# Kernel tuning notes

Measured on AMD Instinct MI355X. Metric: run time of the kernel, lower is better.

Reference implementation:

```python
import jax, jax.numpy as jnp
import numpy as np

VOCAB = 100000
EMBED_DIM = 300
TOPK = 10
BATCH = 1024


def setup_inputs() -> dict:
    key = jax.random.key(0)
    k1, k2 = jax.random.split(key)
    wordid = jax.random.randint(k1, (BATCH,), 0, VOCAB, dtype=jnp.int64 if jax.config.jax_enable_x64 else jnp.int32)
    weight = jax.random.normal(k2, (VOCAB, EMBED_DIM), dtype=jnp.float32)
    return {"wordid": wordid, "weight": weight}


def reference(wordid, weight):
    # Embedding lookup: [B, D]
    wordvec = weight[wordid]
    # Dense similarity against full vocab: [B, V]
    sim = jnp.einsum('bd,vd->bv', wordvec, weight)
    # top-(k+1), sorted descending; drop column 0 (the query word itself)
    score, indice = jax.lax.top_k(sim, TOPK + 1)
    return score[:, 1:], indice[:, 1:]
```

## Files before the change

kernel.cpp:

```cpp
#include <hip/hip_runtime.h>
#include <math.h>

#define BATCH 1024
#define VOCAB 100000
#define KDIM  300
#define TOPK  10

#define NKB    10
#define NCB_B  6272
#define NCB_A  64
#define NCC    392
#define NCAND  (NCC*8)
#define NKF    24
#define NDOT   (NKF*4)

typedef __attribute__((ext_vector_type(8))) short bf16x8;
typedef __attribute__((ext_vector_type(4))) float f32x4;
typedef unsigned long long u64;

#define GL2LDS(gsrc, ldst)                                                    \
    __builtin_amdgcn_global_load_lds(                                         \
        (const __attribute__((address_space(1))) void*)(gsrc),                \
        (__attribute__((address_space(3))) void*)(ldst), 16, 0, 0)

__device__ __forceinline__ ushort f2bf(float f) {
    union { float f; unsigned u; } v; v.f = f;
    unsigned r = v.u + 0x7FFFu + ((v.u >> 16) & 1u);
    return (ushort)(r >> 16);
}

__device__ __forceinline__ void ins4(int (&l)[4], int e) {
    if (e <= l[3]) return;
    bool g0 = e > l[0], g1 = e > l[1], g2 = e > l[2];
    l[3] = g2 ? l[2] : e;
    l[2] = g2 ? (g1 ? l[1] : e) : l[2];
    l[1] = g1 ? (g0 ? l[0] : e) : l[1];
    l[0] = g0 ? e : l[0];
}

template<int N>
__device__ __forceinline__ void pins64(u64 (&ks)[N], u64 k) {
    if (k <= ks[N-1]) return;
    #pragma unroll
    for (int p = N-1; p >= 0; --p) {
        bool gt  = k > ks[p];
        bool gtp = (p > 0) ? (k > ks[p-1]) : false;
        ks[p] = gt ? (gtp ? ks[p-1] : k) : ks[p];
    }
}

__global__ __launch_bounds__(256)
void convert_frags(const int* __restrict__ wordid, const float* __restrict__ weight,
                   ushort* __restrict__ ws_b, ushort* __restrict__ ws_a, int nb4)
{
    const int t   = threadIdx.x;
    const int w   = t >> 6, l = t & 63;
    const int bid = blockIdx.x;
    const bool is_a = (bid >= nb4);
    const int cb  = (is_a ? (bid - nb4) : bid) * 4 + w;
    ushort* dst = is_a ? ws_a : ws_b;
    const int kstride = is_a ? 64 : NCB_B;

    const int r16  = l & 15;
    const int ksub = (l >> 4) * 8;

    const int row = is_a ? wordid[cb*16 + r16] : (cb*16 + r16);
    const bool vr = (row < VOCAB);
    const float* src = weight + (size_t)(vr ? row : 0) * KDIM;

    #pragma unroll
    for (int kb = 0; kb < NKB; ++kb) {
        const int k0 = kb*32 + ksub;
        float4 a = make_float4(0.f,0.f,0.f,0.f);
        float4 b = make_float4(0.f,0.f,0.f,0.f);
        if (vr) {
            if (k0 + 8 <= KDIM) {
                a = *reinterpret_cast<const float4*>(src + k0);
                b = *reinterpret_cast<const float4*>(src + k0 + 4);
            } else if (k0 + 4 <= KDIM) {
                a = *reinterpret_cast<const float4*>(src + k0);
            }
        }
        uint4 o;
        o.x = (unsigned)f2bf(a.x) | ((unsigned)f2bf(a.y) << 16);
        o.y = (unsigned)f2bf(a.z) | ((unsigned)f2bf(a.w) << 16);
        o.z = (unsigned)f2bf(b.x) | ((unsigned)f2bf(b.y) << 16);
        o.w = (unsigned)f2bf(b.z) | ((unsigned)f2bf(b.w) << 16);
        *reinterpret_cast<uint4*>(&dst[((size_t)kb*kstride + cb)*512 + (size_t)l*8]) = o;
    }
}

__global__ __launch_bounds__(512, 2)
void sim_gemm(const ushort* __restrict__ ws_a, const ushort* __restrict__ ws_b,
              unsigned* __restrict__ cand)
{
    __shared__ __align__(16) char pool[131072];

    const int id = blockIdx.x;
    const int cc = (id & 7) + ((id >> 5) << 3);
    const int rc = (id >> 3) & 3;

    const int t    = threadIdx.x;
    const int wid  = t >> 6, lane = t & 63;
    const int wm   = wid >> 2, wn = wid & 3;
    const int l16  = lane & 15, lk = lane >> 4;

    auto stage_slot = [&](int kt, int slot, int buf) {
        char* ldst = pool + buf*65536 + slot*1024;
        const ushort* src;
        if (slot < 32) {
            src = ws_a + (((size_t)(kt*2 + (slot>>4))*64) + rc*16 + (slot & 15))*512
                       + (size_t)lane*8;
        } else {
            int s2 = slot - 32;
            src = ws_b + (((size_t)(kt*2 + (s2>>4))*NCB_B) + cc*16 + (s2 & 15))*512
                       + (size_t)lane*8;
        }
        GL2LDS(src, (ushort*)ldst);
    };

    f32x4 acc[8][4] = {};

    #pragma unroll
    for (int j = 0; j < 8; ++j) stage_slot(0, wid*8 + j, 0);
    asm volatile("s_waitcnt vmcnt(0)" ::: "memory");
    __builtin_amdgcn_s_barrier();
    asm volatile("" ::: "memory");

    for (int kt = 0; kt < 5; ++kt) {
        const int buf = kt & 1;
        const ushort* Ab = (const ushort*)(pool + buf*65536);
        const ushort* Bb = (const ushort*)(pool + buf*65536 + 32768);

        if (kt < 4) {
            #pragma unroll
            for (int j = 0; j < 8; ++j)
                stage_slot(kt + 1, wid*8 + j, buf ^ 1);
        }

        bf16x8 bfr[2][4];
        #pragma unroll
        for (int kb = 0; kb < 2; ++kb)
            #pragma unroll
            for (int nf = 0; nf < 4; ++nf)
                bfr[kb][nf] = *reinterpret_cast<const bf16x8*>(
                    Bb + (size_t)(kb*16 + wn*4 + nf)*512 + lane*8);

        #pragma unroll
        for (int p = 0; p < 4; ++p) {
            bf16x8 af[2][2];
            #pragma unroll
            for (int kb = 0; kb < 2; ++kb)
                #pragma unroll
                for (int m2 = 0; m2 < 2; ++m2)
                    af[kb][m2] = *reinterpret_cast<const bf16x8*>(
                        Ab + (size_t)(kb*16 + wm*8 + p*2 + m2)*512 + lane*8);

            __builtin_amdgcn_s_setprio(1);
            #pragma unroll
            for (int m2 = 0; m2 < 2; ++m2)
                #pragma unroll
                for (int nf = 0; nf < 4; ++nf) {
                    acc[p*2+m2][nf] = __builtin_amdgcn_mfma_f32_16x16x32_bf16(
                        bfr[0][nf], af[0][m2], acc[p*2+m2][nf], 0, 0, 0);
                    acc[p*2+m2][nf] = __builtin_amdgcn_mfma_f32_16x16x32_bf16(
                        bfr[1][nf], af[1][m2], acc[p*2+m2][nf], 0, 0, 0);
                }
            __builtin_amdgcn_s_setprio(0);
        }

        if (kt < 4) {
            asm volatile("s_waitcnt vmcnt(0)" ::: "memory");
            __builtin_amdgcn_s_barrier();
            asm volatile("" ::: "memory");
        }
    }

    __syncthreads();
    int* Cls = (int*)pool;
    #pragma unroll
    for (int mf = 0; mf < 8; ++mf) {
        int k0 = 0, k1 = 0;
        #pragma unroll
        for (int nf = 0; nf < 4; ++nf) {
            float qm = fmaxf(fmaxf(acc[mf][nf][0], acc[mf][nf][1]),
                             fmaxf(acc[mf][nf][2], acc[mf][nf][3]));
            int key = (int)((__float_as_uint(qm) & 0xFFFF0000u)
                            | (unsigned)(wn*16 + nf*4 + lk));
            if (key > k0)      { k1 = k0; k0 = key; }
            else if (key > k1) { k1 = key; }
        }
        int row = wm*128 + mf*16 + l16;
        int ent = wn*4 + lk;
        Cls[row*33 + ent*2 + 0] = k0;
        Cls[row*33 + ent*2 + 1] = k1;
    }
    __syncthreads();

    {
        int row  = t >> 1, half = t & 1;
        int ks[4] = {0, 0, 0, 0};
        #pragma unroll
        for (int j = 0; j < 16; ++j)
            ins4(ks, Cls[row*33 + half*16 + j]);
        int grow = rc*256 + row;
        size_t base = (size_t)grow*NCAND + cc*8 + half*4;
        *reinterpret_cast<uint4*>(&cand[base]) =
            make_uint4((unsigned)ks[0], (unsigned)ks[1],
                       (unsigned)ks[2], (unsigned)ks[3]);
    }
}

__global__ __launch_bounds__(256, 4)
void topk_finalize(const unsigned* __restrict__ cand, const int* __restrict__ wordid,
                   const float* __restrict__ weight, float* __restrict__ out)
{
    __shared__ u64    Wv[4*NKF];
    __shared__ int    Qq[NKF];
    __shared__ float  Qrow[304];
    __shared__ double Rs[NDOT];
    __shared__ int    Rc[NDOT];

    const int row  = blockIdx.x;
    const int t    = threadIdx.x;
    const int wid  = t >> 6, lane = t & 63;

    if (t < 75)
        *reinterpret_cast<float4*>(&Qrow[t*4]) =
            *reinterpret_cast<const float4*>(weight + (size_t)wordid[row]*KDIM + t*4);

    u64 a[13];
    #pragma unroll
    for (int i = 0; i < 13; ++i) a[i] = 0ull;

    const unsigned* rc = cand + (size_t)row*NCAND;
    #pragma unroll
    for (int i = 0; i < 13; ++i) {
        int off = i*64 + lane;
        if (off < 784) {
            int c = wid*784 + off;
            unsigned e = rc[c];
            u64 comb = ((u64)(e ^ 0x80000000u) << 32)
                     | (unsigned)(((c >> 3) << 6) | (e & 63u));
            pins64<13>(a, comb);
        }
    }

    u64 mywin = 0ull;
    for (int k = 0; k < NKF; ++k) {
        u64 h = a[0], r = h;
        #pragma unroll
        for (int m = 1; m < 64; m <<= 1) {
            u64 o = __shfl_xor(r, m);
            r = (o > r) ? o : r;
        }
        bool win = (h == r);
        #pragma unroll
        for (int j = 0; j < 12; ++j) a[j] = win ? a[j+1] : a[j];
        a[12] = win ? 0ull : a[12];
        mywin = (lane == k) ? r : mywin;
    }
    if (lane < NKF) Wv[wid*NKF + lane] = mywin;
    __syncthreads();

    if (wid == 0) {
        u64 b0 = Wv[lane];
        u64 b1 = (lane < 32) ? Wv[lane + 64] : 0ull;
        if (b1 > b0) { u64 tmp = b0; b0 = b1; b1 = tmp; }

        u64 fin = 0ull;
        for (int k = 0; k < NKF; ++k) {
            u64 h = b0, r = h;
            #pragma unroll
            for (int m = 1; m < 64; m <<= 1) {
                u64 o = __shfl_xor(r, m);
                r = (o > r) ? o : r;
            }
            bool win = (h == r);
            b0 = win ? b1 : b0;
            b1 = win ? 0ull : b1;
            fin = (lane == k) ? r : fin;
        }
        if (lane < NKF) Qq[lane] = (int)(fin & 0xffffffffull);
    }
    __syncthreads();

    {
        const int g = t >> 4, l = t & 15;
        for (int ci = g; ci < NDOT; ci += 16) {
            const int q   = Qq[ci >> 2];
            const int col = q*4 + (ci & 3);
            const bool valid = (col < VOCAB);
            const float* wr = weight + (size_t)(valid ? col : 0)*KDIM;

            double a0 = 0.0, a1 = 0.0;
            #pragma unroll
            for (int k = 0; k < 4; ++k) {
                int sl = (l + 16*k) * 4;
                float4 qa = *reinterpret_cast<const float4*>(&Qrow[sl]);
                float4 wb = *reinterpret_cast<const float4*>(wr + sl);
                a0 += (double)qa.x * wb.x + (double)qa.z * wb.z;
                a1 += (double)qa.y * wb.y + (double)qa.w * wb.w;
            }
            if (l < 11) {
                int sl = (l + 64) * 4;
                float4 qa = *reinterpret_cast<const float4*>(&Qrow[sl]);
                float4 wb = *reinterpret_cast<const float4*>(wr + sl);
                a0 += (double)qa.x * wb.x + (double)qa.z * wb.z;
                a1 += (double)qa.y * wb.y + (double)qa.w * wb.w;
            }
            double s = a0 + a1;
            #pragma unroll
            for (int m = 1; m < 16; m <<= 1) s += __shfl_xor(s, m);
            if (l == 0) { Rs[ci] = valid ? s : -1e300; Rc[ci] = valid ? col : 0x7fffffff; }
        }
    }
    __syncthreads();

    if (wid == 0) {
        double v0 = -INFINITY, v1 = -INFINITY;
        int    c0 = 0x7fffffff, c1 = 0x7fffffff;
        if (lane < NDOT/2) {
            v0 = Rs[lane*2];     c0 = Rc[lane*2];
            v1 = Rs[lane*2 + 1]; c1 = Rc[lane*2 + 1];
        }
        for (int kk = 0; kk < TOPK + 1; ++kk) {
            bool sel = (v0 > v1) || (v0 == v1 && c0 < c1);
            double bv = sel ? v0 : v1;
            int    bc = sel ? c0 : c1;
            #pragma unroll
            for (int m = 1; m < 64; m <<= 1) {
                double ov = __shfl_xor(bv, m);
                int    oc = __shfl_xor(bc, m);
                if (ov > bv || (ov == bv && oc < bc)) { bv = ov; bc = oc; }
            }
            if (kk >= 1 && lane == 0) {
                out[(size_t)row*TOPK + (kk-1)] = (float)bv;
                out[(size_t)BATCH*TOPK + (size_t)row*TOPK + (kk-1)] = (float)bc;
            }
            if (c0 == bc) v0 = -INFINITY;
            if (c1 == bc) v1 = -INFINITY;
        }
    }
}

extern "C" void kernel_launch(void* const* d_in, const int* in_sizes, int n_in,
                              void* d_out, int out_size, void* d_ws, size_t ws_size,
                              hipStream_t stream) {
    const int*   wordid = (const int*)d_in[0];
    const float* weight = (const float*)d_in[1];
    float* out = (float*)d_out;

    const size_t SZ_B = (size_t)NCB_B * NKB * 64 * 16;
    const size_t SZ_A = (size_t)NCB_A * NKB * 64 * 16;

    char* p = (char*)d_ws;
    ushort*   ws_b = (ushort*)p;  p += SZ_B;
    ushort*   ws_a = (ushort*)p;  p += SZ_A;
    unsigned* cand = (unsigned*)p;

    convert_frags<<<NCB_B/4 + NCB_A/4, 256, 0, stream>>>(wordid, weight, ws_b, ws_a, NCB_B/4);
    sim_gemm<<<NCC*4, 512, 0, stream>>>(ws_a, ws_b, cand);
    topk_finalize<<<BATCH, 256, 0, stream>>>(cand, wordid, weight, out);
}
```

Before: 155.1 us.

## Run sim_gemm with 1024-thread blocks, halving per-wave M tile

The GEMM block grows from 8 to 16 waves covering the same 256x256 tile, so each wave owns 64 rows instead of 128 and holds half as many accumulators. Staging is split so each wave issues 4 LDS loads per k-step instead of 8, and the epilogue row mapping is adjusted. The aim is more waves to hide LDS and global latency with lower register pressure. The cost is lower per-wave reuse of B fragments, which means more LDS reads per MFMA and heavier barriers. With 128KB of LDS per block, only one block fits per CU, where before there were two 512-thread blocks.

```diff
diff --git a/kernel.cpp b/kernel.cpp
--- a/kernel.cpp
+++ b/kernel.cpp
@@ -90,7 +90,7 @@
     }
 }
 
-__global__ __launch_bounds__(512, 2)
+__global__ __launch_bounds__(1024)
 void sim_gemm(const ushort* __restrict__ ws_a, const ushort* __restrict__ ws_b,
               unsigned* __restrict__ cand)
 {
@@ -105,24 +105,27 @@
     const int wm   = wid >> 2, wn = wid & 3;
     const int l16  = lane & 15, lk = lane >> 4;
 
-    auto stage_slot = [&](int kt, int slot, int buf) {
-        char* ldst = pool + buf*65536 + slot*1024;
-        const ushort* src;
-        if (slot < 32) {
-            src = ws_a + (((size_t)(kt*2 + (slot>>4))*64) + rc*16 + (slot & 15))*512
-                       + (size_t)lane*8;
-        } else {
-            int s2 = slot - 32;
-            src = ws_b + (((size_t)(kt*2 + (s2>>4))*NCB_B) + cc*16 + (s2 & 15))*512
-                       + (size_t)lane*8;
-        }
-        GL2LDS(src, (ushort*)ldst);
+    auto stage = [&](int kt, int buf) {
+        #pragma unroll
+        for (int j = 0; j < 4; ++j) {
+            const int slot = wid*4 + j;
+            char* ldst = pool + buf*65536 + slot*1024;
+            const ushort* src;
+            if (slot < 32) {
+                src = ws_a + ((size_t)(kt*2 + (slot>>4))*64 + rc*16 + (slot & 15))*512
+                           + (size_t)lane*8;
+            } else {
+                int s2 = slot - 32;
+                src = ws_b + ((size_t)(kt*2 + (s2>>4))*NCB_B + cc*16 + (s2 & 15))*512
+                           + (size_t)lane*8;
+            }
+            GL2LDS(src, (ushort*)ldst);
+        }
     };
 
-    f32x4 acc[8][4] = {};
-
-    #pragma unroll
-    for (int j = 0; j < 8; ++j) stage_slot(0, wid*8 + j, 0);
+    f32x4 acc[4][4] = {};
+
+    stage(0, 0);
     asm volatile("s_waitcnt vmcnt(0)" ::: "memory");
     __builtin_amdgcn_s_barrier();
     asm volatile("" ::: "memory");
@@ -132,40 +135,27 @@
         const ushort* Ab = (const ushort*)(pool + buf*65536);
         const ushort* Bb = (const ushort*)(pool + buf*65536 + 32768);
 
-        if (kt < 4) {
-            #pragma unroll
-            for (int j = 0; j < 8; ++j)
-                stage_slot(kt + 1, wid*8 + j, buf ^ 1);
-        }
-
-        bf16x8 bfr[2][4];
-        #pragma unroll
-        for (int kb = 0; kb < 2; ++kb)
+        if (kt < 4) stage(kt + 1, buf ^ 1);
+
+        #pragma unroll
+        for (int kb = 0; kb < 2; ++kb) {
+            bf16x8 bfr[4], af[4];
             #pragma unroll
             for (int nf = 0; nf < 4; ++nf)
-                bfr[kb][nf] = *reinterpret_cast<const bf16x8*>(
+                bfr[nf] = *reinterpret_cast<const bf16x8*>(
                     Bb + (size_t)(kb*16 + wn*4 + nf)*512 + lane*8);
-
-        #pragma unroll
-        for (int p = 0; p < 4; ++p) {
-            bf16x8 af[2][2];
-            #pragma unroll
-            for (int kb = 0; kb < 2; ++kb)
+            #pragma unroll
+            for (int mf = 0; mf < 4; ++mf)
+                af[mf] = *reinterpret_cast<const bf16x8*>(
+                    Ab + (size_t)(kb*16 + wm*4 + mf)*512 + lane*8);
+
+            __builtin_amdgcn_s_setprio(1);
+            #pragma unroll
+            for (int mf = 0; mf < 4; ++mf)
                 #pragma unroll
-                for (int m2 = 0; m2 < 2; ++m2)
-                    af[kb][m2] = *reinterpret_cast<const bf16x8*>(
-                        Ab + (size_t)(kb*16 + wm*8 + p*2 + m2)*512 + lane*8);
-
-            __builtin_amdgcn_s_setprio(1);
-            #pragma unroll
-            for (int m2 = 0; m2 < 2; ++m2)
-                #pragma unroll
-                for (int nf = 0; nf < 4; ++nf) {
-                    acc[p*2+m2][nf] = __builtin_amdgcn_mfma_f32_16x16x32_bf16(
-                        bfr[0][nf], af[0][m2], acc[p*2+m2][nf], 0, 0, 0);
-                    acc[p*2+m2][nf] = __builtin_amdgcn_mfma_f32_16x16x32_bf16(
-                        bfr[1][nf], af[1][m2], acc[p*2+m2][nf], 0, 0, 0);
-                }
+                for (int nf = 0; nf < 4; ++nf)
+                    acc[mf][nf] = __builtin_amdgcn_mfma_f32_16x16x32_bf16(
+                        bfr[nf], af[mf], acc[mf][nf], 0, 0, 0);
             __builtin_amdgcn_s_setprio(0);
         }
 
@@ -179,7 +169,7 @@
     __syncthreads();
     int* Cls = (int*)pool;
     #pragma unroll
-    for (int mf = 0; mf < 8; ++mf) {
+    for (int mf = 0; mf < 4; ++mf) {
         int k0 = 0, k1 = 0;
         #pragma unroll
         for (int nf = 0; nf < 4; ++nf) {
@@ -190,14 +180,14 @@
             if (key > k0)      { k1 = k0; k0 = key; }
             else if (key > k1) { k1 = key; }
         }
-        int row = wm*128 + mf*16 + l16;
+        int row = wm*64 + mf*16 + l16;
         int ent = wn*4 + lk;
         Cls[row*33 + ent*2 + 0] = k0;
         Cls[row*33 + ent*2 + 1] = k1;
     }
     __syncthreads();
 
-    {
+    if (t < 512) {
         int row  = t >> 1, half = t & 1;
         int ks[4] = {0, 0, 0, 0};
         #pragma unroll
@@ -360,6 +350,6 @@
     unsigned* cand = (unsigned*)p;
 
     convert_frags<<<NCB_B/4 + NCB_A/4, 256, 0, stream>>>(wordid, weight, ws_b, ws_a, NCB_B/4);
-    sim_gemm<<<NCC*4, 512, 0, stream>>>(ws_a, ws_b, cand);
+    sim_gemm<<<NCC*4, 1024, 0, stream>>>(ws_a, ws_b, cand);
     topk_finalize<<<BATCH, 256, 0, stream>>>(cand, wordid, weight, out);
 }
```

Result: slower. 190.0 us (+22.5%).
